# Optimization experiments

Hardware: AMD Instinct MI355X
Metric: run time of the kernel (lower is better)

The kernel has to match this reference:

```python
import jax, jax.numpy as jnp
import numpy as np


def _squash(t):
    # squash along axis=2 (the atoms axis of [B, D, A, 1, 1])
    norm = jnp.linalg.norm(t, axis=2, keepdims=True)
    n2 = norm * norm
    return t / norm * (n2 / (1.0 + n2))


def setup_inputs() -> dict:
    key = jax.random.key(0)
    k1, k2 = jax.random.split(key)
    B, I, Ain, D, A = 32, 2048, 16, 32, 16
    x = jax.random.normal(k1, (B, I, Ain, 1, 1), jnp.float32)
    weights = 0.1 * jax.random.normal(k2, (I, Ain, D * A, 1, 1), jnp.float32)
    bias = jnp.full((D, A, 1, 1), 0.1, jnp.float32)  # nn.init.constant_(0.1)
    return {"x": x, "weights": weights, "bias": bias, "num_routing": 3}


def reference(x, weights, bias, num_routing):
    B, I, Ain = x.shape[:3]
    D, A = bias.shape[:2]
    # Vote computation (standard voting): sum over input_atoms.
    # Torch does expand+mul+sum; einsum is the same math without the 4.8GB intermediate.
    votes = jnp.einsum('bia,iao->bio', x[:, :, :, 0, 0],
                       weights[:, :, :, 0, 0]).reshape(B, I, D, A, 1, 1)
    votes_sg = jax.lax.stop_gradient(votes)  # votes_trans_stopped in torch
    logits = jnp.zeros((B, I, D, 1, 1), x.dtype)
    activation = None
    for i in range(num_routing):
        route = jax.nn.softmax(logits, axis=2)  # [B, I, D, 1, 1], softmax over D
        v = votes if i == num_routing - 1 else votes_sg
        # route broadcast over atoms axis; sum over input capsules I
        preact = jnp.sum(route[:, :, :, None] * v, axis=1) + bias  # [B, D, A, 1, 1]
        activation = _squash(preact)
        if i < num_routing - 1:
            # agreement update uses non-stopped votes (as in torch)
            logits = logits + jnp.sum(votes * activation[:, None], axis=3)  # [B, I, D, 1, 1]
    return activation
```

## Files before the change

kernel.cpp:

```cpp
#include <hip/hip_runtime.h>


#define B_  32
#define I_  2048
#define K_  16
#define O_  512
#define NG_ 256
#define IC_ 8

#define GLB(p)  ((const __attribute__((address_space(1))) void*)(p))
#define LDSP(p) ((__attribute__((address_space(3))) void*)(p))

template<int PASS>
__global__ __launch_bounds__(256, 2)
void sweep_kernel(const float* __restrict__ x, const float* __restrict__ W,
                  const float* __restrict__ act0_g, const float* __restrict__ act1_g,
                  float* __restrict__ partial)
{
    const int tid  = threadIdx.x;
    const int lane = tid & 63;
    const int wave = tid >> 6;
    const int bid  = blockIdx.x;
    const int ig   = (bid & 7) * 32 + (bid >> 4);
    const int bh   = (bid >> 3) & 1;
    const int d    = lane >> 1;
    const int h    = lane & 1;
    const int obase = d * 16 + h * 8;

    const int wv    = __builtin_amdgcn_readfirstlane(wave);
    const int bbase = bh * 16 + wv * 4;

    __shared__ float sW[2][K_ * O_];

    int voff[8];
    #pragma unroll
    for (int c = 0; c < 8; ++c) {
        const int s = c * 256 + wave * 64 + lane;
        const int f = ((s >> 10) & 1) | ((s & 1) << 1)
                    | (((s >> 1) & 31) << 2) | (((s >> 6) & 15) << 7);
        voff[c] = f << 4;
    }

    float facc[4][8];
    #pragma unroll
    for (int bb = 0; bb < 4; ++bb)
        #pragma unroll
        for (int j = 0; j < 8; ++j) facc[bb][j] = 0.f;

    float a0[4][8], a1[4][8];
    if (PASS >= 1) {
        #pragma unroll
        for (int bb = 0; bb < 4; ++bb) {
            const float4* p = (const float4*)(act0_g + (bbase + bb) * O_ + obase);
            float4 f0 = p[0], f1 = p[1];
            a0[bb][0]=f0.x; a0[bb][1]=f0.y; a0[bb][2]=f0.z; a0[bb][3]=f0.w;
            a0[bb][4]=f1.x; a0[bb][5]=f1.y; a0[bb][6]=f1.z; a0[bb][7]=f1.w;
        }
    }
    if (PASS == 2) {
        #pragma unroll
        for (int bb = 0; bb < 4; ++bb) {
            const float4* p = (const float4*)(act1_g + (bbase + bb) * O_ + obase);
            float4 f0 = p[0], f1 = p[1];
            a1[bb][0]=f0.x; a1[bb][1]=f0.y; a1[bb][2]=f0.z; a1[bb][3]=f0.w;
            a1[bb][4]=f1.x; a1[bb][5]=f1.y; a1[bb][6]=f1.z; a1[bb][7]=f1.w;
        }
    }

    {
        const char* gb = (const char*)(W + (size_t)(ig * IC_) * (K_ * O_));
        #pragma unroll
        for (int c = 0; c < 8; ++c)
            __builtin_amdgcn_global_load_lds(GLB(gb + voff[c]),
                LDSP(&sW[0][(c * 256 + wave * 64) * 4]), 16, 0, 0);
    }

    #pragma unroll 1
    for (int ii = 0; ii < IC_; ++ii) {
        const int i = ig * IC_ + ii;
        __syncthreads();
        if (ii + 1 < IC_) {
            const char* gb = (const char*)(W + (size_t)(i + 1) * (K_ * O_));
            float* nbuf = sW[(ii + 1) & 1];
            #pragma unroll
            for (int c = 0; c < 8; ++c)
                __builtin_amdgcn_global_load_lds(GLB(gb + voff[c]),
                    LDSP(&nbuf[(c * 256 + wave * 64) * 4]), 16, 0, 0);
        }
        const float* cbuf = sW[ii & 1];

        float xs[4][16];
        #pragma unroll
        for (int bb = 0; bb < 4; ++bb) {
            const float4* xp = (const float4*)(x + ((size_t)(bbase + bb) * I_ + i) * K_);
            #pragma unroll
            for (int q = 0; q < 4; ++q) {
                float4 v = xp[q];
                xs[bb][4*q+0]=v.x; xs[bb][4*q+1]=v.y; xs[bb][4*q+2]=v.z; xs[bb][4*q+3]=v.w;
            }
        }

        float V[4][8];
        #pragma unroll
        for (int bb = 0; bb < 4; ++bb)
            #pragma unroll
            for (int j = 0; j < 8; ++j) V[bb][j] = 0.f;
        #pragma unroll
        for (int k = 0; k < K_; ++k) {
            const float4 w0 = *(const float4*)&cbuf[k * 256 + lane * 4];
            const float4 w1 = *(const float4*)&cbuf[4096 + k * 256 + lane * 4];
            const float w[8] = {w0.x, w0.y, w0.z, w0.w, w1.x, w1.y, w1.z, w1.w};
            #pragma unroll
            for (int bb = 0; bb < 4; ++bb) {
                const float xb = xs[bb][k];
                #pragma unroll
                for (int j = 0; j < 8; ++j) V[bb][j] = fmaf(xb, w[j], V[bb][j]);
            }
        }

        #pragma unroll
        for (int bb = 0; bb < 4; ++bb) {
            if (PASS == 0) {
                #pragma unroll
                for (int j = 0; j < 8; ++j) facc[bb][j] += V[bb][j];
            } else {
                float p0 = 0.f;
                #pragma unroll
                for (int j = 0; j < 8; ++j) p0 = fmaf(V[bb][j], a0[bb][j], p0);
                p0 += __shfl_xor(p0, 1);
                float lg = p0;
                if (PASS == 2) {
                    float p1 = 0.f;
                    #pragma unroll
                    for (int j = 0; j < 8; ++j) p1 = fmaf(V[bb][j], a1[bb][j], p1);
                    p1 += __shfl_xor(p1, 1);
                    lg += p1;
                }
                const float e = __expf(lg);
                float s = e;
                s += __shfl_xor(s, 2);
                s += __shfl_xor(s, 4);
                s += __shfl_xor(s, 8);
                s += __shfl_xor(s, 16);
                s += __shfl_xor(s, 32);
                const float r = e * __builtin_amdgcn_rcpf(s);
                #pragma unroll
                for (int j = 0; j < 8; ++j)
                    facc[bb][j] = fmaf(r, V[bb][j], facc[bb][j]);
            }
        }
    }

    #pragma unroll
    for (int bb = 0; bb < 4; ++bb) {
        const int b = bbase + bb;
        float4* dst = (float4*)(partial + ((size_t)ig * B_ + b) * O_ + obase);
        dst[0] = make_float4(facc[bb][0], facc[bb][1], facc[bb][2], facc[bb][3]);
        dst[1] = make_float4(facc[bb][4], facc[bb][5], facc[bb][6], facc[bb][7]);
    }
}

__global__ __launch_bounds__(256)
void reduce_squash(const float* __restrict__ partial, const float* __restrict__ bias,
                   float scale, float* __restrict__ out)
{
    const int t  = threadIdx.x;
    const int g  = blockIdx.x * 32 + (t & 31);
    const int sl = t >> 5;
    float s = 0.f;
    #pragma unroll
    for (int w = sl * 32; w < sl * 32 + 32; ++w)
        s += partial[(size_t)w * (B_ * O_) + g];
    __shared__ float red[256];
    red[t] = s;
    __syncthreads();
    if (t < 32) {
        float v = red[t];
        #pragma unroll
        for (int r = 1; r < 8; ++r) v += red[t + 32 * r];
        const float p = fmaf(v, scale, bias[g & (O_ - 1)]);
        float nn = p * p;
        nn += __shfl_xor(nn, 1);
        nn += __shfl_xor(nn, 2);
        nn += __shfl_xor(nn, 4);
        nn += __shfl_xor(nn, 8);
        out[g] = p * sqrtf(nn) / (1.f + nn);
    }
}

extern "C" void kernel_launch(void* const* d_in, const int* in_sizes, int n_in,
                              void* d_out, int out_size, void* d_ws, size_t ws_size,
                              hipStream_t stream) {
    const float* x    = (const float*)d_in[0];
    const float* W    = (const float*)d_in[1];
    const float* bias = (const float*)d_in[2];
    float* out = (float*)d_out;

    float* partial = (float*)d_ws;
    float* act0    = partial + (size_t)NG_ * B_ * O_;
    float* act1    = act0 + B_ * O_;

    sweep_kernel<0><<<NG_ * 2, 256, 0, stream>>>(x, W, nullptr, nullptr, partial);
    reduce_squash<<<512, 256, 0, stream>>>(partial, bias, 1.f / 32.f, act0);
    sweep_kernel<1><<<NG_ * 2, 256, 0, stream>>>(x, W, act0, nullptr, partial);
    reduce_squash<<<512, 256, 0, stream>>>(partial, bias, 1.f, act1);
    sweep_kernel<2><<<NG_ * 2, 256, 0, stream>>>(x, W, act0, act1, partial);
    reduce_squash<<<512, 256, 0, stream>>>(partial, bias, 1.f, out);
}
```

Baseline: 188.8 us.

## Cover all batches per block and merge activation vectors for logits

Each block now handles all 32 batches (8 per wave) over 4 input capsules, instead of 16 batches over 8 capsules. Each weight tile loaded into LDS is therefore reused across twice as many batches, which halves total W traffic from global memory. In passes 1 and 2 the two activation vectors are summed once up front, so the logit is one dot product instead of two. The trade is more registers per thread and more partial buffers for the reduction to sum (512 instead of 256), which could lower occupancy and lengthen the reduce kernel.

New measurement: 256.7 us. 1.36x slower.

```diff
diff --git a/kernel.cpp b/kernel.cpp
--- a/kernel.cpp
+++ b/kernel.cpp
@@ -5,8 +5,8 @@
 #define I_  2048
 #define K_  16
 #define O_  512
-#define NG_ 256
-#define IC_ 8
+#define NG_ 512
+#define IC_ 4
 
 #define GLB(p)  ((const __attribute__((address_space(1))) void*)(p))
 #define LDSP(p) ((__attribute__((address_space(3))) void*)(p))
@@ -20,15 +20,13 @@
     const int tid  = threadIdx.x;
     const int lane = tid & 63;
     const int wave = tid >> 6;
-    const int bid  = blockIdx.x;
-    const int ig   = (bid & 7) * 32 + (bid >> 4);
-    const int bh   = (bid >> 3) & 1;
+    const int ig   = blockIdx.x;
     const int d    = lane >> 1;
     const int h    = lane & 1;
     const int obase = d * 16 + h * 8;
 
     const int wv    = __builtin_amdgcn_readfirstlane(wave);
-    const int bbase = bh * 16 + wv * 4;
+    const int bbase = wv * 8;
 
     __shared__ float sW[2][K_ * O_];
 
@@ -41,29 +39,26 @@
         voff[c] = f << 4;
     }
 
-    float facc[4][8];
+    float facc[8][8];
     #pragma unroll
-    for (int bb = 0; bb < 4; ++bb)
+    for (int bb = 0; bb < 8; ++bb)
         #pragma unroll
         for (int j = 0; j < 8; ++j) facc[bb][j] = 0.f;
 
-    float a0[4][8], a1[4][8];
+    float as_[8][8];
     if (PASS >= 1) {
         #pragma unroll
-        for (int bb = 0; bb < 4; ++bb) {
+        for (int bb = 0; bb < 8; ++bb) {
             const float4* p = (const float4*)(act0_g + (bbase + bb) * O_ + obase);
             float4 f0 = p[0], f1 = p[1];
-            a0[bb][0]=f0.x; a0[bb][1]=f0.y; a0[bb][2]=f0.z; a0[bb][3]=f0.w;
-            a0[bb][4]=f1.x; a0[bb][5]=f1.y; a0[bb][6]=f1.z; a0[bb][7]=f1.w;
-        }
-    }
-    if (PASS == 2) {
-        #pragma unroll
-        for (int bb = 0; bb < 4; ++bb) {
-            const float4* p = (const float4*)(act1_g + (bbase + bb) * O_ + obase);
-            float4 f0 = p[0], f1 = p[1];
-            a1[bb][0]=f0.x; a1[bb][1]=f0.y; a1[bb][2]=f0.z; a1[bb][3]=f0.w;
-            a1[bb][4]=f1.x; a1[bb][5]=f1.y; a1[bb][6]=f1.z; a1[bb][7]=f1.w;
+            as_[bb][0]=f0.x; as_[bb][1]=f0.y; as_[bb][2]=f0.z; as_[bb][3]=f0.w;
+            as_[bb][4]=f1.x; as_[bb][5]=f1.y; as_[bb][6]=f1.z; as_[bb][7]=f1.w;
+            if (PASS == 2) {
+                const float4* q = (const float4*)(act1_g + (bbase + bb) * O_ + obase);
+                float4 g0 = q[0], g1 = q[1];
+                as_[bb][0]+=g0.x; as_[bb][1]+=g0.y; as_[bb][2]+=g0.z; as_[bb][3]+=g0.w;
+                as_[bb][4]+=g1.x; as_[bb][5]+=g1.y; as_[bb][6]+=g1.z; as_[bb][7]+=g1.w;
+            }
         }
     }
 
@@ -89,54 +84,44 @@
         }
         const float* cbuf = sW[ii & 1];
 
-        float xs[4][16];
+        float V[8][8];
         #pragma unroll
-        for (int bb = 0; bb < 4; ++bb) {
-            const float4* xp = (const float4*)(x + ((size_t)(bbase + bb) * I_ + i) * K_);
-            #pragma unroll
-            for (int q = 0; q < 4; ++q) {
-                float4 v = xp[q];
-                xs[bb][4*q+0]=v.x; xs[bb][4*q+1]=v.y; xs[bb][4*q+2]=v.z; xs[bb][4*q+3]=v.w;
-            }
-        }
-
-        float V[4][8];
-        #pragma unroll
-        for (int bb = 0; bb < 4; ++bb)
+        for (int bb = 0; bb < 8; ++bb)
             #pragma unroll
             for (int j = 0; j < 8; ++j) V[bb][j] = 0.f;
+
         #pragma unroll
-        for (int k = 0; k < K_; ++k) {
-            const float4 w0 = *(const float4*)&cbuf[k * 256 + lane * 4];
-            const float4 w1 = *(const float4*)&cbuf[4096 + k * 256 + lane * 4];
-            const float w[8] = {w0.x, w0.y, w0.z, w0.w, w1.x, w1.y, w1.z, w1.w};
+        for (int kc = 0; kc < 4; ++kc) {
+            float4 xc[8];
             #pragma unroll
-            for (int bb = 0; bb < 4; ++bb) {
-                const float xb = xs[bb][k];
+            for (int bb = 0; bb < 8; ++bb)
+                xc[bb] = *(const float4*)(x + ((size_t)(bbase + bb) * I_ + i) * K_ + kc * 4);
+            #pragma unroll
+            for (int kq = 0; kq < 4; ++kq) {
+                const int k = kc * 4 + kq;
+                const float4 w0 = *(const float4*)&cbuf[k * 256 + lane * 4];
+                const float4 w1 = *(const float4*)&cbuf[4096 + k * 256 + lane * 4];
+                const float w[8] = {w0.x, w0.y, w0.z, w0.w, w1.x, w1.y, w1.z, w1.w};
                 #pragma unroll
-                for (int j = 0; j < 8; ++j) V[bb][j] = fmaf(xb, w[j], V[bb][j]);
+                for (int bb = 0; bb < 8; ++bb) {
+                    const float xb = ((const float*)&xc[bb])[kq];
+                    #pragma unroll
+                    for (int j = 0; j < 8; ++j) V[bb][j] = fmaf(xb, w[j], V[bb][j]);
+                }
             }
         }
 
         #pragma unroll
-        for (int bb = 0; bb < 4; ++bb) {
+        for (int bb = 0; bb < 8; ++bb) {
             if (PASS == 0) {
                 #pragma unroll
                 for (int j = 0; j < 8; ++j) facc[bb][j] += V[bb][j];
             } else {
                 float p0 = 0.f;
                 #pragma unroll
-                for (int j = 0; j < 8; ++j) p0 = fmaf(V[bb][j], a0[bb][j], p0);
+                for (int j = 0; j < 8; ++j) p0 = fmaf(V[bb][j], as_[bb][j], p0);
                 p0 += __shfl_xor(p0, 1);
-                float lg = p0;
-                if (PASS == 2) {
-                    float p1 = 0.f;
-                    #pragma unroll
-                    for (int j = 0; j < 8; ++j) p1 = fmaf(V[bb][j], a1[bb][j], p1);
-                    p1 += __shfl_xor(p1, 1);
-                    lg += p1;
-                }
-                const float e = __expf(lg);
+                const float e = __expf(p0);
                 float s = e;
                 s += __shfl_xor(s, 2);
                 s += __shfl_xor(s, 4);
@@ -152,7 +137,7 @@
     }
 
     #pragma unroll
-    for (int bb = 0; bb < 4; ++bb) {
+    for (int bb = 0; bb < 8; ++bb) {
         const int b = bbase + bb;
         float4* dst = (float4*)(partial + ((size_t)ig * B_ + b) * O_ + obase);
         dst[0] = make_float4(facc[bb][0], facc[bb][1], facc[bb][2], facc[bb][3]);
@@ -168,8 +153,8 @@
     const int g  = blockIdx.x * 32 + (t & 31);
     const int sl = t >> 5;
     float s = 0.f;
-    #pragma unroll
-    for (int w = sl * 32; w < sl * 32 + 32; ++w)
+    #pragma unroll 8
+    for (int w = sl * 64; w < sl * 64 + 64; ++w)
         s += partial[(size_t)w * (B_ * O_) + g];
     __shared__ float red[256];
     red[t] = s;
@@ -200,10 +185,10 @@
     float* act0    = partial + (size_t)NG_ * B_ * O_;
     float* act1    = act0 + B_ * O_;
 
-    sweep_kernel<0><<<NG_ * 2, 256, 0, stream>>>(x, W, nullptr, nullptr, partial);
+    sweep_kernel<0><<<NG_, 256, 0, stream>>>(x, W, nullptr, nullptr, partial);
     reduce_squash<<<512, 256, 0, stream>>>(partial, bias, 1.f / 32.f, act0);
-    sweep_kernel<1><<<NG_ * 2, 256, 0, stream>>>(x, W, act0, nullptr, partial);
+    sweep_kernel<1><<<NG_, 256, 0, stream>>>(x, W, act0, nullptr, partial);
     reduce_squash<<<512, 256, 0, stream>>>(partial, bias, 1.f, act1);
-    sweep_kernel<2><<<NG_ * 2, 256, 0, stream>>>(x, W, act0, act1, partial);
+    sweep_kernel<2><<<NG_, 256, 0, stream>>>(x, W, act0, act1, partial);
     reduce_squash<<<512, 256, 0, stream>>>(partial, bias, 1.f, out);
 }
```

## Single-buffer W in LDS, halve I-chunk, raise occupancy, merge activations

Applied to the files above, without the earlier changes.

Halves per-block LDS by switching the W tile from double to single buffering. Each block now covers 4 input capsules instead of 8 across twice as many groups, and the launch-bounds occupancy hint goes from 2 to 4 blocks per CU. In pass 2 the two activation vectors are summed once up front, so only one dot product is needed per iteration. The trade-off is losing load/compute overlap within a block, relying on more resident blocks to hide latency, and doubling the partial buffer that reduce_squash must sum.

Result: slower. 436.5 us (+131.2%).

```diff
diff --git a/kernel.cpp b/kernel.cpp
--- a/kernel.cpp
+++ b/kernel.cpp
@@ -5,14 +5,14 @@
 #define I_  2048
 #define K_  16
 #define O_  512
-#define NG_ 256
-#define IC_ 8
+#define NG_ 512
+#define IC_ 4
 
 #define GLB(p)  ((const __attribute__((address_space(1))) void*)(p))
 #define LDSP(p) ((__attribute__((address_space(3))) void*)(p))
 
 template<int PASS>
-__global__ __launch_bounds__(256, 2)
+__global__ __launch_bounds__(256, 4)
 void sweep_kernel(const float* __restrict__ x, const float* __restrict__ W,
                   const float* __restrict__ act0_g, const float* __restrict__ act1_g,
                   float* __restrict__ partial)
@@ -21,7 +21,7 @@
     const int lane = tid & 63;
     const int wave = tid >> 6;
     const int bid  = blockIdx.x;
-    const int ig   = (bid & 7) * 32 + (bid >> 4);
+    const int ig   = (bid & 7) * 64 + (bid >> 4);
     const int bh   = (bid >> 3) & 1;
     const int d    = lane >> 1;
     const int h    = lane & 1;
@@ -30,7 +30,7 @@
     const int wv    = __builtin_amdgcn_readfirstlane(wave);
     const int bbase = bh * 16 + wv * 4;
 
-    __shared__ float sW[2][K_ * O_];
+    __shared__ float sW[K_ * O_];
 
     int voff[8];
     #pragma unroll
@@ -47,23 +47,20 @@
         #pragma unroll
         for (int j = 0; j < 8; ++j) facc[bb][j] = 0.f;
 
-    float a0[4][8], a1[4][8];
+    float as_[4][8];
     if (PASS >= 1) {
         #pragma unroll
         for (int bb = 0; bb < 4; ++bb) {
             const float4* p = (const float4*)(act0_g + (bbase + bb) * O_ + obase);
             float4 f0 = p[0], f1 = p[1];
-            a0[bb][0]=f0.x; a0[bb][1]=f0.y; a0[bb][2]=f0.z; a0[bb][3]=f0.w;
-            a0[bb][4]=f1.x; a0[bb][5]=f1.y; a0[bb][6]=f1.z; a0[bb][7]=f1.w;
-        }
-    }
-    if (PASS == 2) {
-        #pragma unroll
-        for (int bb = 0; bb < 4; ++bb) {
-            const float4* p = (const float4*)(act1_g + (bbase + bb) * O_ + obase);
-            float4 f0 = p[0], f1 = p[1];
-            a1[bb][0]=f0.x; a1[bb][1]=f0.y; a1[bb][2]=f0.z; a1[bb][3]=f0.w;
-            a1[bb][4]=f1.x; a1[bb][5]=f1.y; a1[bb][6]=f1.z; a1[bb][7]=f1.w;
+            as_[bb][0]=f0.x; as_[bb][1]=f0.y; as_[bb][2]=f0.z; as_[bb][3]=f0.w;
+            as_[bb][4]=f1.x; as_[bb][5]=f1.y; as_[bb][6]=f1.z; as_[bb][7]=f1.w;
+            if (PASS == 2) {
+                const float4* q = (const float4*)(act1_g + (bbase + bb) * O_ + obase);
+                float4 g0 = q[0], g1 = q[1];
+                as_[bb][0]+=g0.x; as_[bb][1]+=g0.y; as_[bb][2]+=g0.z; as_[bb][3]+=g0.w;
+                as_[bb][4]+=g1.x; as_[bb][5]+=g1.y; as_[bb][6]+=g1.z; as_[bb][7]+=g1.w;
+            }
         }
     }
 
@@ -72,22 +69,12 @@
         #pragma unroll
         for (int c = 0; c < 8; ++c)
             __builtin_amdgcn_global_load_lds(GLB(gb + voff[c]),
-                LDSP(&sW[0][(c * 256 + wave * 64) * 4]), 16, 0, 0);
+                LDSP(&sW[(c * 256 + wave * 64) * 4]), 16, 0, 0);
     }
 
     #pragma unroll 1
     for (int ii = 0; ii < IC_; ++ii) {
         const int i = ig * IC_ + ii;
-        __syncthreads();
-        if (ii + 1 < IC_) {
-            const char* gb = (const char*)(W + (size_t)(i + 1) * (K_ * O_));
-            float* nbuf = sW[(ii + 1) & 1];
-            #pragma unroll
-            for (int c = 0; c < 8; ++c)
-                __builtin_amdgcn_global_load_lds(GLB(gb + voff[c]),
-                    LDSP(&nbuf[(c * 256 + wave * 64) * 4]), 16, 0, 0);
-        }
-        const float* cbuf = sW[ii & 1];
 
         float xs[4][16];
         #pragma unroll
@@ -100,6 +87,8 @@
             }
         }
 
+        __syncthreads();
+
         float V[4][8];
         #pragma unroll
         for (int bb = 0; bb < 4; ++bb)
@@ -107,8 +96,8 @@
             for (int j = 0; j < 8; ++j) V[bb][j] = 0.f;
         #pragma unroll
         for (int k = 0; k < K_; ++k) {
-            const float4 w0 = *(const float4*)&cbuf[k * 256 + lane * 4];
-            const float4 w1 = *(const float4*)&cbuf[4096 + k * 256 + lane * 4];
+            const float4 w0 = *(const float4*)&sW[k * 256 + lane * 4];
+            const float4 w1 = *(const float4*)&sW[4096 + k * 256 + lane * 4];
             const float w[8] = {w0.x, w0.y, w0.z, w0.w, w1.x, w1.y, w1.z, w1.w};
             #pragma unroll
             for (int bb = 0; bb < 4; ++bb) {
@@ -116,6 +105,15 @@
                 #pragma unroll
                 for (int j = 0; j < 8; ++j) V[bb][j] = fmaf(xb, w[j], V[bb][j]);
             }
+        }
+
+        if (ii + 1 < IC_) {
+            __syncthreads();
+            const char* gb = (const char*)(W + (size_t)(i + 1) * (K_ * O_));
+            #pragma unroll
+            for (int c = 0; c < 8; ++c)
+                __builtin_amdgcn_global_load_lds(GLB(gb + voff[c]),
+                    LDSP(&sW[(c * 256 + wave * 64) * 4]), 16, 0, 0);
         }
 
         #pragma unroll
@@ -126,17 +124,9 @@
             } else {
                 float p0 = 0.f;
                 #pragma unroll
-                for (int j = 0; j < 8; ++j) p0 = fmaf(V[bb][j], a0[bb][j], p0);
+                for (int j = 0; j < 8; ++j) p0 = fmaf(V[bb][j], as_[bb][j], p0);
                 p0 += __shfl_xor(p0, 1);
-                float lg = p0;
-                if (PASS == 2) {
-                    float p1 = 0.f;
-                    #pragma unroll
-                    for (int j = 0; j < 8; ++j) p1 = fmaf(V[bb][j], a1[bb][j], p1);
-                    p1 += __shfl_xor(p1, 1);
-                    lg += p1;
-                }
-                const float e = __expf(lg);
+                const float e = __expf(p0);
                 float s = e;
                 s += __shfl_xor(s, 2);
                 s += __shfl_xor(s, 4);
@@ -168,8 +158,8 @@
     const int g  = blockIdx.x * 32 + (t & 31);
     const int sl = t >> 5;
     float s = 0.f;
-    #pragma unroll
-    for (int w = sl * 32; w < sl * 32 + 32; ++w)
+    #pragma unroll 8
+    for (int w = sl * 64; w < sl * 64 + 64; ++w)
         s += partial[(size_t)w * (B_ * O_) + g];
     __shared__ float red[256];
     red[t] = s;
```
